# Kernel optimization log

Hardware: AMD Instinct MI355X
Metric: run time of the kernel (lower is better)

## Reference

```python
import jax, jax.numpy as jnp
import numpy as np

# LIF hyperparameters (from the torch module's `parameters` dict)
C = 1.0            # C_Osc
THR = 1.0          # v_Osc_threshold
BS = 256           # trials_per_stimulus
N = 512            # neurons_n
N_IN = 512         # n_in
TAU_SYN = 0.01     # tau_Osc_Ie
TAU_SYN_REC = 0.01 # tau_Osc_Irec
TAU_NEU = 0.02     # tau_Osc
GAIN_SYN = 1.0     # TDE_to_Osc_current
GAIN_SYN_REC = 0.5 # gain_syn_rec
DT = 0.001         # clock_sim
VR = 0.0           # reset_osc
I_MIN = 0.0        # I_minimum_osc
I_STEP = 0.01      # I_step_osc
REFRAC = 0.002     # refrac_Osc
REFR = REFRAC / DT # refractory period in steps
T = 500            # simulated timesteps


def spike(x):
    # SurrGradSpike.forward: hard threshold (surrogate grad only matters in bwd)
    return (x > 0.0).astype(x.dtype)


def setup_inputs() -> dict:
    key = jax.random.key(0)
    k1, k2, k3 = jax.random.split(key, 3)
    x = jax.random.uniform(k1, (T, BS, N_IN), dtype=jnp.float32)
    # train=True init: h1 ~ N(1, (std*0.5/sqrt(n_in))^2), r1 ~ N(0, same)
    std = 1.0 * 0.5 / np.sqrt(N_IN)
    h1 = 1.0 + std * jax.random.normal(k2, (N_IN, N), dtype=jnp.float32)
    r1 = std * jax.random.normal(k3, (N, N), dtype=jnp.float32)
    return {"x": x, "h1": h1, "r1": r1}


def reference(x, h1, r1):
    steady = I_MIN + I_STEP * jnp.arange(N, dtype=jnp.float32)  # [N]

    def step(state, x_t):
        V, Isyn, Irec, cnt, spk = state
        Isyn = Isyn - DT * Isyn / TAU_SYN + GAIN_SYN * (x_t @ h1)
        Irec = Irec - DT * Irec / TAU_SYN_REC + GAIN_SYN_REC * (spk @ r1)
        V = V + DT * (-V / TAU_NEU + (Isyn + Irec + steady) / C)
        V = jnp.maximum(V, 0.0)
        spk_new = spike(V - THR)
        cnt = REFR * spk_new + (1.0 - spk_new) * (cnt - 1.0)
        V = (1.0 - spk_new) * V * (cnt <= 0.0).astype(V.dtype) + spk_new * VR
        return (V, Isyn, Irec, cnt, spk_new), spk_new

    init = (
        jnp.ones((BS, N), jnp.float32),   # V
        jnp.zeros((BS, N), jnp.float32),  # Isyn
        jnp.zeros((BS, N), jnp.float32),  # Irec
        jnp.zeros((BS, N), jnp.float32),  # count_refr
        jnp.zeros((BS, N), jnp.float32),  # spk
    )
    _, spikes = jax.lax.scan(step, init, x)
    return spikes  # [T, BS, N]
```

## Files before the change

kernel.cpp:

```cpp
#include <hip/hip_runtime.h>

typedef __attribute__((ext_vector_type(8))) short short8;
typedef __attribute__((ext_vector_type(4))) float f32x4;

constexpr int BSZ = 256;
constexpr int NRN = 512;
constexpr int KIN = 512;
constexpr int TT  = 500;
constexpr int BM  = 128;
constexpr int BN  = 128;
constexpr int KT  = 32;
constexpr int NBLK = (TT * BSZ / BM) * (NRN / BN);
constexpr size_t WS_NEED = (size_t)2 * KIN * NRN * sizeof(unsigned short);
constexpr unsigned long long FULLM = 0xFFFFFFFFFFFFFFFFULL;

__device__ __forceinline__ unsigned short bf16rne(float f) {
    unsigned u = __float_as_uint(f);
    u += 0x7FFFu + ((u >> 16) & 1u);
    return (unsigned short)(u >> 16);
}
__device__ __forceinline__ float bf16f(unsigned short s) {
    return __uint_as_float(((unsigned)s) << 16);
}
__device__ __forceinline__ unsigned cvtpk(float a, float b) {
    unsigned r;
    asm("v_cvt_pk_bf16_f32 %0, %1, %2" : "=v"(r) : "v"(a), "v"(b));
    return r;
}

__global__ __launch_bounds__(512)
void split_h(const float* __restrict__ h1,
             unsigned short* __restrict__ wsH,
             unsigned short* __restrict__ wsL)
{
    const int k = blockIdx.x;
    const int n = threadIdx.x;
    const float v = h1[(size_t)k * NRN + n];
    const unsigned short h  = bf16rne(v);
    const unsigned short lo = bf16rne(v - bf16f(h));
    const int kt = k >> 5, koct = (k >> 3) & 3, i = k & 7;
    const int nb = n >> 7, nl = n & 127;
    const int byte = (kt * 4 + nb) * 8192 +
                     ((nl * 64 + koct * 16) ^ (((nl >> 1) & 3) << 4)) + i * 2;
    *reinterpret_cast<unsigned short*>((char*)wsH + byte) = h;
    *reinterpret_cast<unsigned short*>((char*)wsL + byte) = lo;
}

template<bool PS>
__global__ __launch_bounds__(256)
void lif_gemm(const float* __restrict__ x,
              const float* __restrict__ h1,
              const unsigned short* __restrict__ wsH,
              const unsigned short* __restrict__ wsL,
              float* __restrict__ out)
{
    __shared__ short AhS[BM * KT], AlS[BM * KT], BhS[BN * KT], BlS[BN * KT];

    const int tid  = threadIdx.x;
    const int l    = tid & 63;
    const int w    = tid >> 6;
    const int wm   = (w & 1) * 64;
    const int wn   = (w >> 1) * 64;
    const int lrow = l & 15;
    const int loct = l >> 4;

    const int nid = (blockIdx.x & 7) * (NBLK / 8) + (blockIdx.x >> 3);
    const size_t m0 = (size_t)(nid >> 2) * BM;
    const int    nb = nid & 3;
    const int    n0 = nb * BN;

    f32x4 acc[4][4];
    #pragma unroll
    for (int i = 0; i < 4; ++i)
        #pragma unroll
        for (int j = 0; j < 4; ++j) acc[i][j] = (f32x4)0.0f;

    for (int kt = 0; kt < KIN / KT; ++kt) {
        if (PS) {
            const float4* sH = reinterpret_cast<const float4*>(
                (const char*)wsH + (kt * 4 + nb) * 8192);
            const float4* sL = reinterpret_cast<const float4*>(
                (const char*)wsL + (kt * 4 + nb) * 8192);
            float4* dH = reinterpret_cast<float4*>(BhS);
            float4* dL = reinterpret_cast<float4*>(BlS);
            dH[tid]       = sH[tid];
            dH[256 + tid] = sH[256 + tid];
            dL[tid]       = sL[tid];
            dL[256 + tid] = sL[256 + tid];
        } else {
            #pragma unroll
            for (int u2 = 0; u2 < 2; ++u2) {
                const int u = u2 * 256 + tid;
                const int nl = u & 127, koct = u >> 7;
                short8 hh, hl;
                #pragma unroll
                for (int i = 0; i < 8; ++i) {
                    const float v = h1[(size_t)(kt * KT + koct * 8 + i) * NRN + n0 + nl];
                    const unsigned short h = bf16rne(v);
                    hh[i] = (short)h;
                    hl[i] = (short)bf16rne(v - bf16f(h));
                }
                const int byte = (nl * 64 + koct * 16) ^ (((nl >> 1) & 3) << 4);
                *reinterpret_cast<short8*>((char*)BhS + byte) = hh;
                *reinterpret_cast<short8*>((char*)BlS + byte) = hl;
            }
        }
        #pragma unroll
        for (int u4 = 0; u4 < 4; ++u4) {
            const int u = u4 * 256 + tid;
            const int row = u >> 3, slot = u & 7;
            const float4 xv = *reinterpret_cast<const float4*>(
                x + (m0 + row) * KIN + kt * KT + slot * 4);
            const unsigned h01 = cvtpk(xv.x, xv.y);
            const unsigned h23 = cvtpk(xv.z, xv.w);
            const float r0 = xv.x - __uint_as_float(h01 << 16);
            const float r1v = xv.y - __uint_as_float(h01 & 0xFFFF0000u);
            const float r2 = xv.z - __uint_as_float(h23 << 16);
            const float r3 = xv.w - __uint_as_float(h23 & 0xFFFF0000u);
            const unsigned l01 = cvtpk(r0, r1v);
            const unsigned l23 = cvtpk(r2, r3);
            const unsigned long long hb = (unsigned long long)h01 | ((unsigned long long)h23 << 32);
            const unsigned long long lb = (unsigned long long)l01 | ((unsigned long long)l23 << 32);
            const int byte = (row * 64 + slot * 8) ^ (((row >> 1) & 3) << 4);
            *reinterpret_cast<unsigned long long*>((char*)AhS + byte) = hb;
            *reinterpret_cast<unsigned long long*>((char*)AlS + byte) = lb;
        }
        __syncthreads();

        short8 ah[4], al[4], bh[4], bl[4];
        #pragma unroll
        for (int mi = 0; mi < 4; ++mi) {
            const int row  = wm + mi * 16 + lrow;
            const int byte = (row * 64 + loct * 16) ^ (((row >> 1) & 3) << 4);
            ah[mi] = *reinterpret_cast<const short8*>((const char*)AhS + byte);
            al[mi] = *reinterpret_cast<const short8*>((const char*)AlS + byte);
        }
        #pragma unroll
        for (int ni = 0; ni < 4; ++ni) {
            const int nn   = wn + ni * 16 + lrow;
            const int byte = (nn * 64 + loct * 16) ^ (((nn >> 1) & 3) << 4);
            bh[ni] = *reinterpret_cast<const short8*>((const char*)BhS + byte);
            bl[ni] = *reinterpret_cast<const short8*>((const char*)BlS + byte);
        }

        __builtin_amdgcn_s_setprio(1);
        #pragma unroll
        for (int mi = 0; mi < 4; ++mi)
            #pragma unroll
            for (int ni = 0; ni < 4; ++ni) {
                acc[mi][ni] = __builtin_amdgcn_mfma_f32_16x16x32_bf16(ah[mi], bh[ni], acc[mi][ni], 0, 0, 0);
                acc[mi][ni] = __builtin_amdgcn_mfma_f32_16x16x32_bf16(ah[mi], bl[ni], acc[mi][ni], 0, 0, 0);
                acc[mi][ni] = __builtin_amdgcn_mfma_f32_16x16x32_bf16(al[mi], bh[ni], acc[mi][ni], 0, 0, 0);
            }
        __builtin_amdgcn_s_setprio(0);
        __syncthreads();
    }

    #pragma unroll
    for (int mi = 0; mi < 4; ++mi)
        #pragma unroll
        for (int j = 0; j < 4; ++j) {
            const size_t row = m0 + wm + mi * 16 + loct * 4 + j;
            float* op = out + row * NRN + n0 + wn + lrow;
            #pragma unroll
            for (int ni = 0; ni < 4; ++ni)
                op[ni * 16] = acc[mi][ni][j];
        }
}

__global__ __launch_bounds__(512, 2)
void lif_scan(const float* __restrict__ r1,
              float* __restrict__ out)
{
    __shared__ unsigned long long smask[2][8];
    __shared__ unsigned long long flg[2];
    __shared__ unsigned long long vflg;

    const int n  = threadIdx.x;
    const int b  = blockIdx.x;
    const int wv = n >> 6;
    const int ln = n & 63;
    const size_t row = (size_t)b * NRN + n;
    constexpr size_t STEP = (size_t)BSZ * NRN;

    if (n < 16) ((unsigned long long*)smask)[n] = 0ULL;
    if (n < 2)  flg[n] = 0ULL;

    double csum = 0.0;
    for (int j = 0; j < KIN; ++j)
        csum += (double)r1[(size_t)j * NRN + n];

    double V = 1.0, Is = 0.0, Ir = 0.0, cnt = 0.0;
    const double steady = 0.01 * (double)n;
    constexpr double kS = 0.1, kN = 0.05, DT = 0.001;

    float cur[8], nxt[8];
    #pragma unroll
    for (int i = 0; i < 8; ++i) cur[i] = out[(size_t)i * STEP + row];
    __syncthreads();

#define STD_STEP(T, AREG)                                                     \
    {                                                                         \
        const int t_ = (T);                                                   \
        const int p_ = t_ & 1;                                                \
        const unsigned long long f_ = flg[p_];                                \
        double aR;                                                            \
        if (f_ == FULLM) {                                                    \
            aR = csum;                                                        \
        } else if (f_ == 0ULL) {                                              \
            aR = 0.0;                                                         \
        } else {                                                              \
            aR = 0.0;                                                         \
            _Pragma("unroll")                                                 \
            for (int w = 0; w < 8; ++w) {                                     \
                unsigned long long m_ = smask[p_][w];                         \
                while (m_) {                                 \
                    const int j = w * 64 + __builtin_ctzll(m_);               \
                    aR += (double)r1[(size_t)j * NRN + n];                    \
                    m_ &= m_ - 1;                                             \
                }                                                             \
            }                                                                 \
        }                                                                     \
        Is = Is - kS * Is + (double)(AREG);                 \
        Ir = Ir - kS * Ir + 0.5 * aR;                       \
        double Vn = V - kN * V + DT * (Is + Ir + steady);                     \
        Vn = fmax(Vn, 0.0);                                                   \
        const bool sp = (Vn - 1.0) > 0.0;                                     \
        cnt = sp ? 2.0 : (cnt - 1.0);                           \
        V = sp ? 0.0 : ((cnt <= 0.0) ? Vn : 0.0);                             \
        out[(size_t)t_ * STEP + row] = sp ? 1.0f : 0.0f;                      \
        const unsigned long long bal = __ballot(sp);                          \
        if (ln == 0) {                                                        \
            smask[p_ ^ 1][wv] = bal;                                          \
            const unsigned char fb =                                          \
                (bal == FULLM) ? 0xFFu : ((bal == 0ULL) ? 0x00u : 0x01u);     \
            ((unsigned char*)&flg[p_ ^ 1])[wv] = fb;                          \
        }                                                                     \
        __syncthreads();                                                      \
    }

    for (int t0 = 0; t0 < 496; t0 += 8) {
        #pragma unroll
        for (int i = 0; i < 8; ++i)
            nxt[i] = (t0 + 8 + i < TT) ? out[(size_t)(t0 + 8 + i) * STEP + row] : 0.0f;

        if (flg[t0 & 1] == FULLM) {
            const double Vc = V, Isc = Is, Irc = Ir, cc = cnt;
            bool allm = true;
            #pragma unroll
            for (int i = 0; i < 8; ++i) {
                Is = Is - kS * Is + (double)cur[i];
                Ir = Ir - kS * Ir + 0.5 * csum;
                double Vn = V - kN * V + DT * (Is + Ir + steady);
                Vn = fmax(Vn, 0.0);
                const bool sp = (Vn - 1.0) > 0.0;
                allm &= sp;
                cnt = sp ? 2.0 : (cnt - 1.0);
                V = sp ? 0.0 : ((cnt <= 0.0) ? Vn : 0.0);
                out[(size_t)(t0 + i) * STEP + row] = sp ? 1.0f : 0.0f;
            }
            const unsigned long long bal = __ballot(allm);
            if (ln == 0) {
                ((unsigned char*)&vflg)[wv] = (bal == FULLM) ? 0xFFu : 0x00u;
                smask[t0 & 1][wv] = FULLM;
                ((unsigned char*)&flg[t0 & 1])[wv] = 0xFFu;
            }
            __syncthreads();
            if (vflg != FULLM) {
                V = Vc; Is = Isc; Ir = Irc; cnt = cc;
                STD_STEP(t0 + 0, cur[0])
                STD_STEP(t0 + 1, cur[1])
                STD_STEP(t0 + 2, cur[2])
                STD_STEP(t0 + 3, cur[3])
                STD_STEP(t0 + 4, cur[4])
                STD_STEP(t0 + 5, cur[5])
                STD_STEP(t0 + 6, cur[6])
                STD_STEP(t0 + 7, cur[7])
            }
        } else {
            STD_STEP(t0 + 0, cur[0])
            STD_STEP(t0 + 1, cur[1])
            STD_STEP(t0 + 2, cur[2])
            STD_STEP(t0 + 3, cur[3])
            STD_STEP(t0 + 4, cur[4])
            STD_STEP(t0 + 5, cur[5])
            STD_STEP(t0 + 6, cur[6])
            STD_STEP(t0 + 7, cur[7])
        }

        #pragma unroll
        for (int i = 0; i < 8; ++i) cur[i] = nxt[i];
    }

    STD_STEP(496, cur[0])
    STD_STEP(497, cur[1])
    STD_STEP(498, cur[2])
    STD_STEP(499, cur[3])
#undef STD_STEP
}

extern "C" void kernel_launch(void* const* d_in, const int* in_sizes, int n_in,
                              void* d_out, int out_size, void* d_ws, size_t ws_size,
                              hipStream_t stream) {
    const float* x  = (const float*)d_in[0];
    const float* h1 = (const float*)d_in[1];
    const float* r1 = (const float*)d_in[2];
    float* out = (float*)d_out;
    (void)in_sizes; (void)n_in; (void)out_size;

    if (ws_size >= WS_NEED) {
        unsigned short* wsH = (unsigned short*)d_ws;
        unsigned short* wsL = wsH + (size_t)KIN * NRN;
        split_h<<<dim3(KIN), dim3(NRN), 0, stream>>>(h1, wsH, wsL);
        lif_gemm<true><<<dim3(NBLK), dim3(256), 0, stream>>>(x, h1, wsH, wsL, out);
    } else {
        lif_gemm<false><<<dim3(NBLK), dim3(256), 0, stream>>>(x, h1, nullptr, nullptr, out);
    }
    lif_scan<<<dim3(BSZ), dim3(512), 0, stream>>>(r1, out);
}
```

Before: 335.7 us.

## Restructure input GEMM to full-width 64-row tiles reading B fragments from global

Replaces the 128x128-tile GEMM with a 512-thread kernel where each block computes a 64-row by full 512-column tile, so each x row block is loaded and split into bf16 hi/lo exactly once instead of four times. The pre-split weights are stored in a new MFMA-fragment layout and read directly from global memory (L2-cached) into registers, removing the B shared-memory staging and its barrier traffic. The trade-off is heavier per-thread global loads of B and more accumulator registers (16 fragments) per wave, with occupancy constrained by launch bounds of 4 blocks.

```diff
diff --git a/kernel.cpp b/kernel.cpp
--- a/kernel.cpp
+++ b/kernel.cpp
@@ -7,9 +7,11 @@
 constexpr int NRN = 512;
 constexpr int KIN = 512;
 constexpr int TT  = 500;
+constexpr int KT  = 32;
+constexpr int BM2 = 64;
+constexpr int NB2 = TT * BSZ / BM2;
 constexpr int BM  = 128;
 constexpr int BN  = 128;
-constexpr int KT  = 32;
 constexpr int NBLK = (TT * BSZ / BM) * (NRN / BN);
 constexpr size_t WS_NEED = (size_t)2 * KIN * NRN * sizeof(unsigned short);
 constexpr unsigned long long FULLM = 0xFFFFFFFFFFFFFFFFULL;
@@ -38,21 +40,101 @@
     const float v = h1[(size_t)k * NRN + n];
     const unsigned short h  = bf16rne(v);
     const unsigned short lo = bf16rne(v - bf16f(h));
-    const int kt = k >> 5, koct = (k >> 3) & 3, i = k & 7;
-    const int nb = n >> 7, nl = n & 127;
-    const int byte = (kt * 4 + nb) * 8192 +
-                     ((nl * 64 + koct * 16) ^ (((nl >> 1) & 3) << 4)) + i * 2;
+    const size_t byte = ((size_t)(k >> 3) * 512 + n) * 16 + (k & 7) * 2;
     *reinterpret_cast<unsigned short*>((char*)wsH + byte) = h;
     *reinterpret_cast<unsigned short*>((char*)wsL + byte) = lo;
 }
 
-template<bool PS>
+__global__ __launch_bounds__(512, 4)
+void lif_gemm2(const float* __restrict__ x,
+               const unsigned short* __restrict__ wsH,
+               const unsigned short* __restrict__ wsL,
+               float* __restrict__ out)
+{
+    __shared__ short AhS[BM2 * KT], AlS[BM2 * KT];
+
+    const int tid  = threadIdx.x;
+    const int l    = tid & 63;
+    const int w    = tid >> 6;
+    const int wm   = (w >> 2) * 32;
+    const int wn   = (w & 3) * 128;
+    const int lrow = l & 15;
+    const int loct = l >> 4;
+
+    const int nid = (blockIdx.x & 7) * (NB2 / 8) + (blockIdx.x >> 3);
+    const size_t m0 = (size_t)nid * BM2;
+
+    const int arow  = tid >> 3;
+    const int aslot = tid & 7;
+    const int abyte = (arow * 64 + aslot * 8) ^ (((arow >> 1) & 3) << 4);
+
+    f32x4 acc[2][8];
+    #pragma unroll
+    for (int i = 0; i < 2; ++i)
+        #pragma unroll
+        for (int j = 0; j < 8; ++j) acc[i][j] = (f32x4)0.0f;
+
+    for (int kt = 0; kt < KIN / KT; ++kt) {
+        {
+            const float4 xv = *reinterpret_cast<const float4*>(
+                x + (m0 + arow) * KIN + kt * KT + aslot * 4);
+            const unsigned h01 = cvtpk(xv.x, xv.y);
+            const unsigned h23 = cvtpk(xv.z, xv.w);
+            const float r0  = xv.x - __uint_as_float(h01 << 16);
+            const float r1v = xv.y - __uint_as_float(h01 & 0xFFFF0000u);
+            const float r2  = xv.z - __uint_as_float(h23 << 16);
+            const float r3  = xv.w - __uint_as_float(h23 & 0xFFFF0000u);
+            const unsigned l01 = cvtpk(r0, r1v);
+            const unsigned l23 = cvtpk(r2, r3);
+            const unsigned long long hb = (unsigned long long)h01 | ((unsigned long long)h23 << 32);
+            const unsigned long long lb = (unsigned long long)l01 | ((unsigned long long)l23 << 32);
+            *reinterpret_cast<unsigned long long*>((char*)AhS + abyte) = hb;
+            *reinterpret_cast<unsigned long long*>((char*)AlS + abyte) = lb;
+        }
+        __syncthreads();
+
+        short8 ah[2], al[2];
+        #pragma unroll
+        for (int mi = 0; mi < 2; ++mi) {
+            const int row  = wm + mi * 16 + lrow;
+            const int byte = (row * 64 + loct * 16) ^ (((row >> 1) & 3) << 4);
+            ah[mi] = *reinterpret_cast<const short8*>((const char*)AhS + byte);
+            al[mi] = *reinterpret_cast<const short8*>((const char*)AlS + byte);
+        }
+
+        __builtin_amdgcn_s_setprio(1);
+        #pragma unroll
+        for (int ni = 0; ni < 8; ++ni) {
+            const size_t bb = ((size_t)(kt * 4 + loct) * 512 + wn + ni * 16 + lrow) * 16;
+            const short8 bh = *reinterpret_cast<const short8*>((const char*)wsH + bb);
+            const short8 bl = *reinterpret_cast<const short8*>((const char*)wsL + bb);
+            #pragma unroll
+            for (int mi = 0; mi < 2; ++mi) {
+                acc[mi][ni] = __builtin_amdgcn_mfma_f32_16x16x32_bf16(ah[mi], bh, acc[mi][ni], 0, 0, 0);
+                acc[mi][ni] = __builtin_amdgcn_mfma_f32_16x16x32_bf16(ah[mi], bl, acc[mi][ni], 0, 0, 0);
+                acc[mi][ni] = __builtin_amdgcn_mfma_f32_16x16x32_bf16(al[mi], bh, acc[mi][ni], 0, 0, 0);
+            }
+        }
+        __builtin_amdgcn_s_setprio(0);
+        __syncthreads();
+    }
+
+    #pragma unroll
+    for (int mi = 0; mi < 2; ++mi)
+        #pragma unroll
+        for (int j = 0; j < 4; ++j) {
+            const size_t row = m0 + wm + mi * 16 + loct * 4 + j;
+            float* op = out + row * NRN + wn + lrow;
+            #pragma unroll
+            for (int ni = 0; ni < 8; ++ni)
+                op[ni * 16] = acc[mi][ni][j];
+        }
+}
+
 __global__ __launch_bounds__(256)
-void lif_gemm(const float* __restrict__ x,
-              const float* __restrict__ h1,
-              const unsigned short* __restrict__ wsH,
-              const unsigned short* __restrict__ wsL,
-              float* __restrict__ out)
+void lif_gemm_fb(const float* __restrict__ x,
+                 const float* __restrict__ h1,
+                 float* __restrict__ out)
 {
     __shared__ short AhS[BM * KT], AlS[BM * KT], BhS[BN * KT], BlS[BN * KT];
 
@@ -66,8 +148,7 @@
 
     const int nid = (blockIdx.x & 7) * (NBLK / 8) + (blockIdx.x >> 3);
     const size_t m0 = (size_t)(nid >> 2) * BM;
-    const int    nb = nid & 3;
-    const int    n0 = nb * BN;
+    const int    n0 = (nid & 3) * BN;
 
     f32x4 acc[4][4];
     #pragma unroll
@@ -76,34 +157,21 @@
         for (int j = 0; j < 4; ++j) acc[i][j] = (f32x4)0.0f;
 
     for (int kt = 0; kt < KIN / KT; ++kt) {
-        if (PS) {
-            const float4* sH = reinterpret_cast<const float4*>(
-                (const char*)wsH + (kt * 4 + nb) * 8192);
-            const float4* sL = reinterpret_cast<const float4*>(
-                (const char*)wsL + (kt * 4 + nb) * 8192);
-            float4* dH = reinterpret_cast<float4*>(BhS);
-            float4* dL = reinterpret_cast<float4*>(BlS);
-            dH[tid]       = sH[tid];
-            dH[256 + tid] = sH[256 + tid];
-            dL[tid]       = sL[tid];
-            dL[256 + tid] = sL[256 + tid];
-        } else {
-            #pragma unroll
-            for (int u2 = 0; u2 < 2; ++u2) {
-                const int u = u2 * 256 + tid;
-                const int nl = u & 127, koct = u >> 7;
-                short8 hh, hl;
-                #pragma unroll
-                for (int i = 0; i < 8; ++i) {
-                    const float v = h1[(size_t)(kt * KT + koct * 8 + i) * NRN + n0 + nl];
-                    const unsigned short h = bf16rne(v);
-                    hh[i] = (short)h;
-                    hl[i] = (short)bf16rne(v - bf16f(h));
-                }
-                const int byte = (nl * 64 + koct * 16) ^ (((nl >> 1) & 3) << 4);
-                *reinterpret_cast<short8*>((char*)BhS + byte) = hh;
-                *reinterpret_cast<short8*>((char*)BlS + byte) = hl;
-            }
+        #pragma unroll
+        for (int u2 = 0; u2 < 2; ++u2) {
+            const int u = u2 * 256 + tid;
+            const int nl = u & 127, koct = u >> 7;
+            short8 hh, hl;
+            #pragma unroll
+            for (int i = 0; i < 8; ++i) {
+                const float v = h1[(size_t)(kt * KT + koct * 8 + i) * NRN + n0 + nl];
+                const unsigned short h = bf16rne(v);
+                hh[i] = (short)h;
+                hl[i] = (short)bf16rne(v - bf16f(h));
+            }
+            const int byte = (nl * 64 + koct * 16) ^ (((nl >> 1) & 3) << 4);
+            *reinterpret_cast<short8*>((char*)BhS + byte) = hh;
+            *reinterpret_cast<short8*>((char*)BlS + byte) = hl;
         }
         #pragma unroll
         for (int u4 = 0; u4 < 4; ++u4) {
@@ -113,10 +181,10 @@
                 x + (m0 + row) * KIN + kt * KT + slot * 4);
             const unsigned h01 = cvtpk(xv.x, xv.y);
             const unsigned h23 = cvtpk(xv.z, xv.w);
-            const float r0 = xv.x - __uint_as_float(h01 << 16);
+            const float r0  = xv.x - __uint_as_float(h01 << 16);
             const float r1v = xv.y - __uint_as_float(h01 & 0xFFFF0000u);
-            const float r2 = xv.z - __uint_as_float(h23 << 16);
-            const float r3 = xv.w - __uint_as_float(h23 & 0xFFFF0000u);
+            const float r2  = xv.z - __uint_as_float(h23 << 16);
+            const float r3  = xv.w - __uint_as_float(h23 & 0xFFFF0000u);
             const unsigned l01 = cvtpk(r0, r1v);
             const unsigned l23 = cvtpk(r2, r3);
             const unsigned long long hb = (unsigned long long)h01 | ((unsigned long long)h23 << 32);
@@ -312,9 +380,9 @@
         unsigned short* wsH = (unsigned short*)d_ws;
         unsigned short* wsL = wsH + (size_t)KIN * NRN;
         split_h<<<dim3(KIN), dim3(NRN), 0, stream>>>(h1, wsH, wsL);
-        lif_gemm<true><<<dim3(NBLK), dim3(256), 0, stream>>>(x, h1, wsH, wsL, out);
+        lif_gemm2<<<dim3(NB2), dim3(512), 0, stream>>>(x, wsH, wsL, out);
     } else {
-        lif_gemm<false><<<dim3(NBLK), dim3(256), 0, stream>>>(x, h1, nullptr, nullptr, out);
+        lif_gemm_fb<<<dim3(NBLK), dim3(256), 0, stream>>>(x, h1, out);
     }
     lif_scan<<<dim3(BSZ), dim3(512), 0, stream>>>(r1, out);
 }
```

Measured after the change: 393.2 us. 17.1% more time.
